# Optimization experiments

Measured on AMD Instinct MI355X. Metric: run time of the kernel, lower is better.

The kernel has to match this reference:

```python
import jax, jax.numpy as jnp
import numpy as np

EPS = 1e-6

def rms_norm(x):
    # x / sqrt(mean(x^2, axis=-1) + eps)
    return x * jax.lax.rsqrt(jnp.mean(x * x, axis=-1, keepdims=True) + EPS)

def setup_inputs() -> dict:
    key = jax.random.key(0)
    k1, k2, k3 = jax.random.split(key, 3)
    T, B, D = 2048, 16, 1024
    x = jax.random.normal(k1, (T, B, D), dtype=jnp.float32)
    h0 = jax.random.normal(k2, (B, D), dtype=jnp.float32)
    # Orthogonal-ish init scaled by 0.5 (faithful to nn.init.orthogonal_ then *0.5)
    A = jax.random.normal(k3, (D, D), dtype=jnp.float32)
    Q, _ = jnp.linalg.qr(A)
    W = 0.5 * Q
    b = jnp.zeros((D,), dtype=jnp.float32)
    log_alpha = jnp.asarray(np.log(0.1), dtype=jnp.float32)
    return {"x": x, "h0": h0, "W": W, "b": b, "log_alpha": log_alpha}

def reference(x, h0, W, b, log_alpha):
    T, B, D = x.shape
    alpha = jnp.exp(log_alpha)
    # Precompute Wx for all timesteps: [T, B, D]
    Wx_all = jnp.einsum('tbd,ed->tbe', x, W) + b

    def step(h_prev, wx_t):
        h_raw = h_prev + alpha * wx_t
        h_new = rms_norm(h_raw)
        out = h_new * jax.nn.silu(h_new)
        return h_new, (h_new, out)

    _, (h_seq, output) = jax.lax.scan(step, h0, Wx_all)
    h = jnp.concatenate([h0[None], h_seq], axis=0)  # [T+1, B, D]
    return output, h
```

## Files before the change

### kernel.cpp

```cpp
#include <hip/hip_runtime.h>
#include <hip/hip_bf16.h>

#define TT 2048
#define BB 16
#define DD 1024
#define BD (BB*DD)
#define MR (TT*BB)
#define EPSV 1e-6f
#define CH 256
#define NCH (TT/CH)
#define RING 8

typedef __bf16 bf16x8_t __attribute__((ext_vector_type(8)));
typedef float  f32x4_t  __attribute__((ext_vector_type(4)));
typedef __attribute__((address_space(1))) void gvoid_t;
typedef __attribute__((address_space(3))) void lvoid_t;

static __device__ __forceinline__ unsigned short f2bf(float f) {
    __hip_bfloat16 h = __float2bfloat16(f);
    return __builtin_bit_cast(unsigned short, h);
}

__global__ void k_convert(const float* __restrict__ x, const float* __restrict__ W,
                          unsigned short* __restrict__ xb, unsigned short* __restrict__ wb) {
    const long NX4 = (long)MR * DD / 4;
    const long NW4 = (long)DD * DD / 4;
    const long stride = (long)gridDim.x * blockDim.x;
    for (long j = (long)blockIdx.x * blockDim.x + threadIdx.x; j < NX4 + NW4; j += stride) {
        const float4* src; unsigned short* dst; long o;
        if (j < NX4) { src = (const float4*)x; dst = xb; o = j; }
        else         { src = (const float4*)W; dst = wb; o = j - NX4; }
        float4 v = src[o];
        ushort4 u;
        u.x = f2bf(v.x); u.y = f2bf(v.y); u.z = f2bf(v.z); u.w = f2bf(v.w);
        *(ushort4*)(dst + o * 4) = u;
    }
}

__global__ __launch_bounds__(256, 2)
void k_gemm(const unsigned short* __restrict__ A, const unsigned short* __restrict__ Bw,
            const float* __restrict__ bias, float* __restrict__ C) {
    __shared__ char lds[16384];
    char* ldsA = lds;
    char* ldsB = lds + 8192;
    const int tid  = threadIdx.x;
    const int lane = tid & 63;
    const int wid  = tid >> 6;
    const int wm = wid >> 1, wn = wid & 1;
    const size_t arow0 = (size_t)blockIdx.y * 128;
    const int    brow0 = blockIdx.x * 128;

    f32x4_t acc[4][4] = {};

    const int off0 = tid * 16,        row0_ = off0 >> 6, colb0 = off0 & 63;
    const int off1 = 4096 + tid * 16, row1_ = off1 >> 6, colb1 = off1 & 63;

    for (int kk = 0; kk < DD / 32; ++kk) {
        const int kbase = kk * 32;
        __builtin_amdgcn_global_load_lds(
            (gvoid_t*)(A + (arow0 + row0_) * DD + kbase + (colb0 >> 1)),
            (lvoid_t*)(ldsA + off0), 16, 0, 0);
        __builtin_amdgcn_global_load_lds(
            (gvoid_t*)(A + (arow0 + row1_) * DD + kbase + (colb1 >> 1)),
            (lvoid_t*)(ldsA + off1), 16, 0, 0);
        __builtin_amdgcn_global_load_lds(
            (gvoid_t*)(Bw + (size_t)(brow0 + row0_) * DD + kbase + (colb0 >> 1)),
            (lvoid_t*)(ldsB + off0), 16, 0, 0);
        __builtin_amdgcn_global_load_lds(
            (gvoid_t*)(Bw + (size_t)(brow0 + row1_) * DD + kbase + (colb1 >> 1)),
            (lvoid_t*)(ldsB + off1), 16, 0, 0);
        __syncthreads();

        const int ml = lane & 15;
        const int kh = (lane >> 4) * 16;
        bf16x8_t av[4], bv[4];
        #pragma unroll
        for (int i = 0; i < 4; ++i) {
            av[i] = *(const bf16x8_t*)(ldsA + (wm * 64 + i * 16 + ml) * 64 + kh);
            bv[i] = *(const bf16x8_t*)(ldsB + (wn * 64 + i * 16 + ml) * 64 + kh);
        }
        #pragma unroll
        for (int i = 0; i < 4; ++i)
            #pragma unroll
            for (int j = 0; j < 4; ++j)
                acc[i][j] = __builtin_amdgcn_mfma_f32_16x16x32_bf16(av[i], bv[j], acc[i][j], 0, 0, 0);
        __syncthreads();
    }

    const int rq = (lane >> 4) * 4;
    const int cl = lane & 15;
    #pragma unroll
    for (int i = 0; i < 4; ++i) {
        #pragma unroll
        for (int j = 0; j < 4; ++j) {
            const int n = brow0 + wn * 64 + j * 16 + cl;
            const float bb = bias[n];
            #pragma unroll
            for (int q = 0; q < 4; ++q) {
                const size_t m = arow0 + wm * 64 + i * 16 + rq + q;
                C[m * DD + n] = acc[i][j][q] + bb;
            }
        }
    }
}

__global__ __launch_bounds__(64, 1)
void k_phaseA(const float* __restrict__ Wx, const float* __restrict__ h0,
              const float* __restrict__ la, float* __restrict__ hout,
              float* __restrict__ rtab) {
    __shared__ float rbuf[TT];
    const int b = blockIdx.x;
    const int lane = threadIdx.x;
    const float alpha = expf(la[0]);
    const int dof = lane * 4;
    const float* wbase = Wx + b * DD + dof;

    float h[16];
    #pragma unroll
    for (int k = 0; k < 4; ++k) {
        float4 v = *(const float4*)(h0 + b * DD + k * 256 + dof);
        h[k*4+0] = v.x; h[k*4+1] = v.y; h[k*4+2] = v.z; h[k*4+3] = v.w;
    }
    asm volatile("" :: "v"(h[0]), "v"(h[1]), "v"(h[2]), "v"(h[3]),
                       "v"(h[4]), "v"(h[5]), "v"(h[6]), "v"(h[7]),
                       "v"(h[8]), "v"(h[9]), "v"(h[10]), "v"(h[11]),
                       "v"(h[12]), "v"(h[13]), "v"(h[14]), "v"(h[15]));

    f32x4_t buf[RING][4];
    #pragma unroll
    for (int s = 0; s < RING; ++s) {
        const float* wp = wbase + (size_t)s * BD;
        #pragma unroll
        for (int k = 0; k < 4; ++k)
            asm volatile("global_load_dwordx4 %0, %1, off"
                         : "=v"(buf[s][k]) : "v"(wp + k * 256));
    }

    for (int tt = 0; tt < TT; tt += RING) {
        #pragma unroll
        for (int s = 0; s < RING; ++s) {
            const int t = tt + s + 1;

            if (((t - 1) & (CH - 1)) == 0) {
                float* hp = hout + (size_t)(t - 1) * BD + b * DD;
                #pragma unroll
                for (int k = 0; k < 4; ++k) {
                    float4 v; v.x = h[k*4+0]; v.y = h[k*4+1]; v.z = h[k*4+2]; v.w = h[k*4+3];
                    *(float4*)(hp + k * 256 + dof) = v;
                }
            }

            asm volatile("s_waitcnt vmcnt(%0)" :: "i"(4 * (RING - 1)) : "memory");
            __builtin_amdgcn_sched_barrier(0);

            float hr[16];
            float s0 = 0.f, s1 = 0.f, s2 = 0.f, s3 = 0.f;
            #pragma unroll
            for (int k = 0; k < 4; ++k) {
                const f32x4_t w = buf[s][k];
                hr[k*4+0] = fmaf(alpha, w[0], h[k*4+0]);
                hr[k*4+1] = fmaf(alpha, w[1], h[k*4+1]);
                hr[k*4+2] = fmaf(alpha, w[2], h[k*4+2]);
                hr[k*4+3] = fmaf(alpha, w[3], h[k*4+3]);
                s0 = fmaf(hr[k*4+0], hr[k*4+0], s0);
                s1 = fmaf(hr[k*4+1], hr[k*4+1], s1);
                s2 = fmaf(hr[k*4+2], hr[k*4+2], s2);
                s3 = fmaf(hr[k*4+3], hr[k*4+3], s3);
            }
            float ss = (s0 + s1) + (s2 + s3);
            asm volatile(
                "s_nop 1\n\t"
                "v_add_f32 %0, %0, %0 row_shr:1 bound_ctrl:0\n\t"
                "s_nop 1\n\t"
                "v_add_f32 %0, %0, %0 row_shr:2 bound_ctrl:0\n\t"
                "s_nop 1\n\t"
                "v_add_f32 %0, %0, %0 row_shr:4 bank_mask:0xe\n\t"
                "s_nop 1\n\t"
                "v_add_f32 %0, %0, %0 row_shr:8 bank_mask:0xc\n\t"
                "s_nop 1\n\t"
                "v_add_f32 %0, %0, %0 row_bcast:15 row_mask:0xa\n\t"
                "s_nop 1\n\t"
                "v_add_f32 %0, %0, %0 row_bcast:31 row_mask:0xc\n\t"
                "s_nop 1"
                : "+v"(ss));
            const float total = __builtin_bit_cast(float,
                                    __builtin_amdgcn_readlane(__builtin_bit_cast(int, ss), 63));
            const float r = __builtin_amdgcn_rsqf(total * (1.0f / DD) + EPSV);
            if (lane == 0) rbuf[t - 1] = r;
            #pragma unroll
            for (int e = 0; e < 16; ++e) h[e] = r * hr[e];

            const float* wp = wbase + (size_t)((t - 1 + RING) & (TT - 1)) * BD;
            #pragma unroll
            for (int k = 0; k < 4; ++k)
                asm volatile("global_load_dwordx4 %0, %1, off"
                             : "=v"(buf[s][k]) : "v"(wp + k * 256));
        }
    }

    asm volatile("s_waitcnt vmcnt(0)" ::: "memory");

    __syncthreads();
    float* rrow = rtab + b * TT;
    #pragma unroll
    for (int i = 0; i < TT / 4 / 64; ++i) {
        const int j = (i * 64 + lane) * 4;
        float4 v; v.x = rbuf[j]; v.y = rbuf[j+1]; v.z = rbuf[j+2]; v.w = rbuf[j+3];
        *(float4*)(rrow + j) = v;
    }
}

__global__ __launch_bounds__(256)
void k_phaseB(float* __restrict__ WxOut, float* __restrict__ hout,
              const float* __restrict__ rtab, const float* __restrict__ la) {
    const int col = blockIdx.x * 256 + threadIdx.x;
    const int c = blockIdx.y;
    const int b = col >> 10;
    const float alpha = expf(la[0]);
    const float* rr = rtab + b * TT;
    float h = hout[(size_t)(c * CH) * BD + col];
    const int t0 = c * CH + 1;
    float w = WxOut[(size_t)(t0 - 1) * BD + col];
    for (int s = 0; s < CH; ++s) {
        const int t = t0 + s;
        float wnext = 0.f;
        if (s + 1 < CH) wnext = WxOut[(size_t)t * BD + col];
        const float r = rr[t - 1];
        const float hraw = fmaf(alpha, w, h);
        const float hn = r * hraw;
        const float sg = 1.0f / (1.0f + __expf(-hn));
        WxOut[(size_t)(t - 1) * BD + col] = hn * hn * sg;
        if ((t & (CH - 1)) != 0 || t == TT)
            hout[(size_t)t * BD + col] = hn;
        h = hn;
        w = wnext;
    }
}

extern "C" void kernel_launch(void* const* d_in, const int* in_sizes, int n_in,
                              void* d_out, int out_size, void* d_ws, size_t ws_size,
                              hipStream_t stream) {
    (void)in_sizes; (void)n_in; (void)out_size; (void)ws_size;
    const float* x    = (const float*)d_in[0];
    const float* h0   = (const float*)d_in[1];
    const float* W    = (const float*)d_in[2];
    const float* bias = (const float*)d_in[3];
    const float* la   = (const float*)d_in[4];

    float* outr = (float*)d_out;
    float* hreg = outr + (size_t)TT * BD;
    unsigned short* xb = (unsigned short*)hreg;
    unsigned short* wb = xb + (size_t)MR * DD;
    float* rtab = (float*)d_ws;

    k_convert<<<2048, 256, 0, stream>>>(x, W, xb, wb);
    k_gemm<<<dim3(DD / 128, MR / 128), 256, 0, stream>>>(xb, wb, bias, outr);
    k_phaseA<<<BB, 64, 0, stream>>>(outr, h0, la, hreg, rtab);
    k_phaseB<<<dim3(BD / 256, NCH), 256, 0, stream>>>(outr, hreg, rtab, la);
}
```

Before: 507.9 us.

## Restructure sequential RMS scan to use precomputed Gram dot products with producer waves

Phase A is rewritten so the serial scan no longer recomputes the full sum of squares each step. Instead it expands ||h_{t-1}+αw_t||² algebraically using the previous norm, one lookahead dot product per step, and precomputed w_t·w_{t+1} and ||w_t||² terms. Two extra producer waves stream Wx rows into a 32-row LDS ring via direct global-to-LDS loads and compute those Gram terms one phase ahead. The single consumer wave keeps h unnormalized, synchronizes with the producers through block barriers every 8 steps, and uses packed FP32 math. This trades a longer, more intricate dependency chain and possible accumulated rounding error for less latency on the serial critical path.

```diff
diff --git a/kernel.cpp b/kernel.cpp
--- a/kernel.cpp
+++ b/kernel.cpp
@@ -7,14 +7,48 @@
 #define BD (BB*DD)
 #define MR (TT*BB)
 #define EPSV 1e-6f
+#define INVD (1.0f/1024.0f)
 #define CH 256
 #define NCH (TT/CH)
-#define RING 8
+#define PH 8
+#define NPH (TT/PH)
+#define NGP (NPH+2)
 
 typedef __bf16 bf16x8_t __attribute__((ext_vector_type(8)));
 typedef float  f32x4_t  __attribute__((ext_vector_type(4)));
+typedef float  f32x2    __attribute__((ext_vector_type(2)));
 typedef __attribute__((address_space(1))) void gvoid_t;
 typedef __attribute__((address_space(3))) void lvoid_t;
+
+union F4 { float4 v; f32x2 h[2]; float f[4]; };
+
+static __device__ __forceinline__ f32x2 pk_mul(f32x2 a, f32x2 b) {
+    f32x2 d; asm("v_pk_mul_f32 %0, %1, %2" : "=v"(d) : "v"(a), "v"(b)); return d;
+}
+static __device__ __forceinline__ f32x2 pk_fma(f32x2 a, f32x2 b, f32x2 c) {
+    f32x2 d; asm("v_pk_fma_f32 %0, %1, %2, %3" : "=v"(d) : "v"(a), "v"(b), "v"(c)); return d;
+}
+static __device__ __forceinline__ f32x2 pk_add(f32x2 a, f32x2 b) {
+    f32x2 d; asm("v_pk_add_f32 %0, %1, %2" : "=v"(d) : "v"(a), "v"(b)); return d;
+}
+static __device__ __forceinline__ float wave_red_sum(float ss) {
+    asm volatile(
+        "s_nop 1\n\t"
+        "v_add_f32 %0, %0, %0 row_shr:1 bound_ctrl:0\n\t"
+        "s_nop 1\n\t"
+        "v_add_f32 %0, %0, %0 row_shr:2 bound_ctrl:0\n\t"
+        "s_nop 1\n\t"
+        "v_add_f32 %0, %0, %0 row_shr:4 bank_mask:0xe\n\t"
+        "s_nop 1\n\t"
+        "v_add_f32 %0, %0, %0 row_shr:8 bank_mask:0xc\n\t"
+        "s_nop 1\n\t"
+        "v_add_f32 %0, %0, %0 row_bcast:15 row_mask:0xa\n\t"
+        "s_nop 1\n\t"
+        "v_add_f32 %0, %0, %0 row_bcast:31 row_mask:0xc\n\t"
+        "s_nop 1"
+        : "+v"(ss));
+    return __builtin_bit_cast(float, __builtin_amdgcn_readlane(__builtin_bit_cast(int, ss), 63));
+}
 
 static __device__ __forceinline__ unsigned short f2bf(float f) {
     __hip_bfloat16 h = __float2bfloat16(f);
@@ -104,109 +138,200 @@
     }
 }
 
-__global__ __launch_bounds__(64, 1)
+__global__ __launch_bounds__(192, 1)
 void k_phaseA(const float* __restrict__ Wx, const float* __restrict__ h0,
               const float* __restrict__ la, float* __restrict__ hout,
               float* __restrict__ rtab) {
-    __shared__ float rbuf[TT];
-    const int b = blockIdx.x;
-    const int lane = threadIdx.x;
+    __shared__ float  ring[32 * DD];
+    __shared__ float2 gqtab[TT];
+    __shared__ float  rbuf[TT];
+
+    const int b    = blockIdx.x;
+    const int tid  = threadIdx.x;
+    const int wid  = tid >> 6;
+    const int lane = tid & 63;
+    const int dof  = lane * 4;
     const float alpha = expf(la[0]);
-    const int dof = lane * 4;
-    const float* wbase = Wx + b * DD + dof;
-
-    float h[16];
-    #pragma unroll
-    for (int k = 0; k < 4; ++k) {
-        float4 v = *(const float4*)(h0 + b * DD + k * 256 + dof);
-        h[k*4+0] = v.x; h[k*4+1] = v.y; h[k*4+2] = v.z; h[k*4+3] = v.w;
-    }
-    asm volatile("" :: "v"(h[0]), "v"(h[1]), "v"(h[2]), "v"(h[3]),
-                       "v"(h[4]), "v"(h[5]), "v"(h[6]), "v"(h[7]),
-                       "v"(h[8]), "v"(h[9]), "v"(h[10]), "v"(h[11]),
-                       "v"(h[12]), "v"(h[13]), "v"(h[14]), "v"(h[15]));
-
-    f32x4_t buf[RING][4];
-    #pragma unroll
-    for (int s = 0; s < RING; ++s) {
-        const float* wp = wbase + (size_t)s * BD;
-        #pragma unroll
-        for (int k = 0; k < 4; ++k)
-            asm volatile("global_load_dwordx4 %0, %1, off"
-                         : "=v"(buf[s][k]) : "v"(wp + k * 256));
-    }
-
-    for (int tt = 0; tt < TT; tt += RING) {
-        #pragma unroll
-        for (int s = 0; s < RING; ++s) {
-            const int t = tt + s + 1;
-
-            if (((t - 1) & (CH - 1)) == 0) {
-                float* hp = hout + (size_t)(t - 1) * BD + b * DD;
-                #pragma unroll
-                for (int k = 0; k < 4; ++k) {
-                    float4 v; v.x = h[k*4+0]; v.y = h[k*4+1]; v.z = h[k*4+2]; v.w = h[k*4+3];
-                    *(float4*)(hp + k * 256 + dof) = v;
-                }
-            }
-
-            asm volatile("s_waitcnt vmcnt(%0)" :: "i"(4 * (RING - 1)) : "memory");
-            __builtin_amdgcn_sched_barrier(0);
-
-            float hr[16];
-            float s0 = 0.f, s1 = 0.f, s2 = 0.f, s3 = 0.f;
-            #pragma unroll
-            for (int k = 0; k < 4; ++k) {
-                const f32x4_t w = buf[s][k];
-                hr[k*4+0] = fmaf(alpha, w[0], h[k*4+0]);
-                hr[k*4+1] = fmaf(alpha, w[1], h[k*4+1]);
-                hr[k*4+2] = fmaf(alpha, w[2], h[k*4+2]);
-                hr[k*4+3] = fmaf(alpha, w[3], h[k*4+3]);
-                s0 = fmaf(hr[k*4+0], hr[k*4+0], s0);
-                s1 = fmaf(hr[k*4+1], hr[k*4+1], s1);
-                s2 = fmaf(hr[k*4+2], hr[k*4+2], s2);
-                s3 = fmaf(hr[k*4+3], hr[k*4+3], s3);
-            }
-            float ss = (s0 + s1) + (s2 + s3);
-            asm volatile(
-                "s_nop 1\n\t"
-                "v_add_f32 %0, %0, %0 row_shr:1 bound_ctrl:0\n\t"
-                "s_nop 1\n\t"
-                "v_add_f32 %0, %0, %0 row_shr:2 bound_ctrl:0\n\t"
-                "s_nop 1\n\t"
-                "v_add_f32 %0, %0, %0 row_shr:4 bank_mask:0xe\n\t"
-                "s_nop 1\n\t"
-                "v_add_f32 %0, %0, %0 row_shr:8 bank_mask:0xc\n\t"
-                "s_nop 1\n\t"
-                "v_add_f32 %0, %0, %0 row_bcast:15 row_mask:0xa\n\t"
-                "s_nop 1\n\t"
-                "v_add_f32 %0, %0, %0 row_bcast:31 row_mask:0xc\n\t"
-                "s_nop 1"
-                : "+v"(ss));
-            const float total = __builtin_bit_cast(float,
-                                    __builtin_amdgcn_readlane(__builtin_bit_cast(int, ss), 63));
-            const float r = __builtin_amdgcn_rsqf(total * (1.0f / DD) + EPSV);
-            if (lane == 0) rbuf[t - 1] = r;
-            #pragma unroll
-            for (int e = 0; e < 16; ++e) h[e] = r * hr[e];
-
-            const float* wp = wbase + (size_t)((t - 1 + RING) & (TT - 1)) * BD;
+
+    f32x2  hraw[8];
+    F4     wU[2][4], wE[2][4];
+    float  eEv[2] = {0.f, 0.f};
+    float2 gq[2] = {};
+    float  vr1 = 1.f, vr2 = 1.f, ss = 0.f;
+    int    su = 2 * DD, se = 4 * DD;
+
+    if (wid > 0) {
+        const int half = wid - 1;
+        #pragma unroll
+        for (int jj = 0; jj < 4; ++jj) {
+            const int row = half * 4 + jj;
             #pragma unroll
             for (int k = 0; k < 4; ++k)
-                asm volatile("global_load_dwordx4 %0, %1, off"
-                             : "=v"(buf[s][k]) : "v"(wp + k * 256));
-        }
-    }
-
-    asm volatile("s_waitcnt vmcnt(0)" ::: "memory");
-
-    __syncthreads();
-    float* rrow = rtab + b * TT;
-    #pragma unroll
-    for (int i = 0; i < TT / 4 / 64; ++i) {
-        const int j = (i * 64 + lane) * 4;
-        float4 v; v.x = rbuf[j]; v.y = rbuf[j+1]; v.z = rbuf[j+2]; v.w = rbuf[j+3];
-        *(float4*)(rrow + j) = v;
+                __builtin_amdgcn_global_load_lds(
+                    (gvoid_t*)(Wx + (size_t)row * BD + b * DD + k * 256 + dof),
+                    (lvoid_t*)(ring + (row & 31) * DD + k * 256), 16, 0, 0);
+        }
+    }
+
+    for (int gp = 0; gp < NGP; ++gp) {
+        if (wid == 0) {
+            if (gp == 1) {
+                #pragma unroll
+                for (int k = 0; k < 4; ++k) {
+                    F4 u; u.v = *(const float4*)(h0 + b * DD + k * 256 + dof);
+                    hraw[2*k] = u.h[0]; hraw[2*k+1] = u.h[1];
+                }
+                F4 rw0[4], rw1[4], rw2[4], rw3[4];
+                #pragma unroll
+                for (int k = 0; k < 4; ++k) {
+                    rw0[k].v = *(const float4*)(ring + 0 * DD + k * 256 + dof);
+                    rw1[k].v = *(const float4*)(ring + 1 * DD + k * 256 + dof);
+                    rw2[k].v = *(const float4*)(ring + 2 * DD + k * 256 + dof);
+                    rw3[k].v = *(const float4*)(ring + 3 * DD + k * 256 + dof);
+                }
+                f32x2 sa = pk_mul(hraw[0], hraw[0]);
+                #pragma unroll
+                for (int p = 1; p < 8; ++p) sa = pk_fma(hraw[p], hraw[p], sa);
+                ss = wave_red_sum(sa.x + sa.y);
+                f32x2 da = pk_mul(hraw[0], rw0[0].h[0]);
+                f32x2 ea = pk_mul(hraw[0], rw1[0].h[0]);
+                #pragma unroll
+                for (int p = 1; p < 8; ++p) {
+                    da = pk_fma(hraw[p], rw0[p>>1].h[p&1], da);
+                    ea = pk_fma(hraw[p], rw1[p>>1].h[p&1], ea);
+                }
+                eEv[0] = alpha * wave_red_sum(da.x + da.y);
+                eEv[1] = alpha * wave_red_sum(ea.x + ea.y);
+                #pragma unroll
+                for (int k = 0; k < 4; ++k) {
+                    wU[0][k] = rw0[k]; wE[0][k] = rw2[k];
+                    wU[1][k] = rw1[k]; wE[1][k] = rw3[k];
+                }
+                su = 2 * DD; se = 4 * DD; vr1 = 1.f; vr2 = 1.f;
+            } else if (gp >= 2) {
+                const int blk = gp - 2;
+                if (blk == 0) {
+                    gq[0].x = 0.0f;        gq[0].y = gqtab[0].y;
+                    gq[1].x = gqtab[0].x;  gq[1].y = gqtab[1].y;
+                }
+                #pragma unroll
+                for (int s = 0; s < PH; ++s) {
+                    const int t  = blk * PH + s + 1;
+                    const int pe = s & 1;
+                    if (s == 0 && (blk & 31) == 0) {
+                        float* hp = hout + (size_t)(t - 1) * BD + b * DD;
+                        f32x2 rr0 = {vr1, vr1};
+                        #pragma unroll
+                        for (int k = 0; k < 4; ++k) {
+                            F4 u;
+                            u.h[0] = pk_mul(rr0, hraw[2*k]);
+                            u.h[1] = pk_mul(rr0, hraw[2*k+1]);
+                            *(float4*)(hp + k * 256 + dof) = u.v;
+                        }
+                    }
+                    const float Dp = fmaf(vr2, eEv[pe], gq[pe].x);
+                    const float u1 = fmaf(vr1, ss, 2.0f * Dp);
+                    ss = fmaf(vr1, u1, gq[pe].y);
+                    const float ms = fmaf(ss, INVD, EPSV);
+                    const float rt = __builtin_amdgcn_rsqf(ms);
+                    if (lane == 0) rbuf[t - 1] = rt;
+                    f32x2 rr1 = {vr1, vr1};
+                    f32x2 aav = {alpha, alpha};
+                    #pragma unroll
+                    for (int p = 0; p < 8; ++p)
+                        hraw[p] = pk_fma(rr1, hraw[p], pk_mul(aav, wU[pe][p>>1].h[p&1]));
+                    f32x2 ea0 = pk_mul(hraw[0], wE[pe][0].h[0]);
+                    f32x2 ea1 = pk_mul(hraw[1], wE[pe][0].h[1]);
+                    f32x2 ea2 = pk_mul(hraw[2], wE[pe][1].h[0]);
+                    f32x2 ea3 = pk_mul(hraw[3], wE[pe][1].h[1]);
+                    ea0 = pk_fma(hraw[4], wE[pe][2].h[0], ea0);
+                    ea1 = pk_fma(hraw[5], wE[pe][2].h[1], ea1);
+                    ea2 = pk_fma(hraw[6], wE[pe][3].h[0], ea2);
+                    ea3 = pk_fma(hraw[7], wE[pe][3].h[1], ea3);
+                    ea0 = pk_add(ea0, ea1); ea2 = pk_add(ea2, ea3);
+                    ea0 = pk_add(ea0, ea2);
+                    eEv[pe] = alpha * wave_red_sum(ea0.x + ea0.y);
+                    #pragma unroll
+                    for (int k = 0; k < 4; ++k)
+                        wU[pe][k].v = *(const float4*)(ring + su + k * 256 + dof);
+                    #pragma unroll
+                    for (int k = 0; k < 4; ++k)
+                        wE[pe][k].v = *(const float4*)(ring + se + k * 256 + dof);
+                    su = (su + DD) & (32 * DD - 1);
+                    se = (se + DD) & (32 * DD - 1);
+                    {
+                        const int gi = (t     < TT - 1) ? t     : TT - 1;
+                        const int qi = (t + 1 < TT - 1) ? t + 1 : TT - 1;
+                        gq[pe].x = gqtab[gi].x;
+                        gq[pe].y = gqtab[qi].y;
+                    }
+                    vr2 = vr1; vr1 = rt;
+                }
+            }
+            __syncthreads();
+        } else {
+            const int half = wid - 1;
+            if (gp >= 1 && gp <= NPH) {
+                const int sC = gp - 1;
+                const int rbase = sC * PH + half * 4;
+                F4 R[5][4];
+                #pragma unroll
+                for (int jj = 0; jj < 5; ++jj)
+                    #pragma unroll
+                    for (int k = 0; k < 4; ++k)
+                        R[jj][k].v = *(const float4*)(ring + ((rbase + jj) & 31) * DD + k * 256 + dof);
+                float red[8];
+                #pragma unroll
+                for (int sI = 0; sI < 4; ++sI) {
+                    float g = 0.f, q = 0.f;
+                    #pragma unroll
+                    for (int k = 0; k < 4; ++k)
+                        #pragma unroll
+                        for (int j = 0; j < 4; ++j) {
+                            const float w0 = R[sI][k].f[j], w1 = R[sI + 1][k].f[j];
+                            g = fmaf(w0, w1, g);
+                            q = fmaf(w0, w0, q);
+                        }
+                    red[sI] = g; red[4 + sI] = q;
+                }
+                #pragma unroll
+                for (int m = 1; m < 64; m <<= 1)
+                    #pragma unroll
+                    for (int k = 0; k < 8; ++k)
+                        red[k] += __shfl_xor(red[k], m, 64);
+                if (lane == 0) {
+                    const float a2 = alpha * alpha;
+                    #pragma unroll
+                    for (int sI = 0; sI < 4; ++sI)
+                        gqtab[rbase + sI] = make_float2(a2 * red[sI], a2 * red[4 + sI]);
+                }
+            }
+            if (gp < NPH - 1) {
+                const int nb = (gp + 1) * PH + half * 4;
+                #pragma unroll
+                for (int jj = 0; jj < 4; ++jj) {
+                    const int row = nb + jj;
+                    #pragma unroll
+                    for (int k = 0; k < 4; ++k)
+                        __builtin_amdgcn_global_load_lds(
+                            (gvoid_t*)(Wx + (size_t)row * BD + b * DD + k * 256 + dof),
+                            (lvoid_t*)(ring + (row & 31) * DD + k * 256), 16, 0, 0);
+                }
+                asm volatile("s_waitcnt vmcnt(16) lgkmcnt(0)" ::: "memory");
+            } else {
+                asm volatile("s_waitcnt vmcnt(0) lgkmcnt(0)" ::: "memory");
+            }
+            __builtin_amdgcn_s_barrier();
+        }
+    }
+
+    if (wid == 0) {
+        float* rrow = rtab + b * TT;
+        #pragma unroll
+        for (int i = 0; i < TT / 4 / 64; ++i) {
+            const int j = (i * 64 + lane) * 4;
+            *(float4*)(rrow + j) = *(const float4*)(rbuf + j);
+        }
     }
 }
 
@@ -255,6 +380,6 @@
 
     k_convert<<<2048, 256, 0, stream>>>(x, W, xb, wb);
     k_gemm<<<dim3(DD / 128, MR / 128), 256, 0, stream>>>(xb, wb, bias, outr);
-    k_phaseA<<<BB, 64, 0, stream>>>(outr, h0, la, hreg, rtab);
+    k_phaseA<<<BB, 192, 0, stream>>>(outr, h0, la, hreg, rtab);
     k_phaseB<<<dim3(BD / 256, NCH), 256, 0, stream>>>(outr, hreg, rtab, la);
 }
```

After: 752.6 us. +48.2%, slower.
